# Optimization experiments

Hardware: AMD Instinct MI355X
Metric: run time of the kernel (lower is better)

## Reference

```python
import math
import jax, jax.numpy as jnp
import numpy as np

B, N, C = 4, 2048, 256
KMAX, RATIO, ITERS, H = 1024, 12.0, 3, 4
TAU, SIG_FLOOR, INIT_SIG_MIX, INIT_OFF, JIT = 1.0, 0.03, 0.1, 0.5, 1e-6
W_KL, W_ENT, W_OCC, W_COL = 0.05, 0.0, 0.5, 0.1
K_USE = min(max(1, math.ceil(N / RATIO)), KMAX)  # 171
EPS = 1e-8


def _sym(M):
    return 0.5 * (M + jnp.swapaxes(M, -1, -2))


def _l2n(x):
    return x / jnp.maximum(jnp.linalg.norm(x, axis=-1, keepdims=True), 1e-12)


def _ln(x, g, b):
    m = x.mean(-1, keepdims=True)
    v = ((x - m) ** 2).mean(-1, keepdims=True)
    return (x - m) / jnp.sqrt(v + 1e-5) * g + b


def setup_inputs():
    key = jax.random.key(0)
    ks = jax.random.split(key, 16)
    s = jax.random.normal(ks[0], (B, N, C), jnp.float32)
    mu = jax.random.normal(ks[1], (B, N, 3), jnp.float32)
    # per-point SPD covariances (Sigma must be PSD for the overlap solve)
    L = jax.random.normal(ks[2], (B, N, 3, 3), jnp.float32) * 0.3
    Sigma = L @ jnp.swapaxes(L, -1, -2) + 0.05 * jnp.eye(3, dtype=jnp.float32)
    mask = jnp.ones((B, N), jnp.float32)
    lim = 1.0 / math.sqrt(C)
    u = lambda k, sh: jax.random.uniform(k, sh, jnp.float32, -lim, lim)
    return dict(
        s=s, mu=mu, Sigma=Sigma, mask=mask,
        slot_embed_pool=jax.random.normal(ks[3], (KMAX, C), jnp.float32) * 0.02,
        geo_offsets_pool=jax.random.normal(ks[4], (KMAX, 3), jnp.float32) * 0.5,
        gating_W=u(ks[5], (C, C)), proj_q_W=u(ks[6], (C, C)), proj_k_W=u(ks[7], (C, C)),
        gru_w_ih=u(ks[8], (3 * C, C)), gru_w_hh=u(ks[9], (3 * C, C)),
        gru_b_ih=u(ks[10], (3 * C,)), gru_b_hh=u(ks[11], (3 * C,)),
        ln_g=jnp.ones((C,), jnp.float32), ln_b=jnp.zeros((C,), jnp.float32),
        mlp_w1=u(ks[12], (4 * C, C)), mlp_b1=u(ks[13], (4 * C,)),
        mlp_w2=u(ks[14], (C, 4 * C)), mlp_b2=u(ks[15], (C,)),
        w_geo=jnp.float32(1.0),
        geo_scale_raw=jnp.full((H,), -4.0, jnp.float32),
        geo_bias=jnp.full((H,), -6.0, jnp.float32),
    )


def _forward(s, mu, Sigma, mask, slot_embed_pool, geo_offsets_pool, gating_W,
             proj_q_W, proj_k_W, gru_w_ih, gru_w_hh, gru_b_ih, gru_b_hh,
             ln_g, ln_b, mlp_w1, mlp_b1, mlp_w2, mlp_b2,
             w_geo, geo_scale_raw, geo_bias):
    I3 = jnp.eye(3, dtype=s.dtype)
    m1 = mask[:, :, None]                    # [B,N,1]
    cnt = jnp.maximum(mask.sum(1), EPS)      # [B]

    # ---- slot selection (eval mode: no gate noise, rand_slots=0) ----
    s_global = (s * m1).sum(1) / cnt[:, None]
    q = _l2n(s_global @ gating_W.T)
    kn = _l2n(slot_embed_pool)
    scores = q @ kn.T                        # [B,KMAX]
    idx = jax.lax.top_k(scores, K_USE)[1]    # [B,K]
    slots = slot_embed_pool[idx]             # [B,K,C]
    geo_off = geo_offsets_pool[idx]          # [B,K,3]

    # ---- masked mean/std of mu ----
    mean = (mu * m1).sum(1) / cnt[:, None]   # [B,3]
    dm = mu - mean[:, None, :]
    cov = jnp.einsum('bni,bnj->bij', dm * m1, dm) / cnt[:, None, None]
    cov = _sym(cov)
    std = jnp.sqrt(jnp.maximum(jnp.diagonal(cov, axis1=-2, axis2=-1), EPS))
    std = jnp.maximum(std, SIG_FLOOR)
    mu_k = mean[:, None, :] + geo_off * (INIT_OFF * std[:, None, :])

    Sig_avg = _sym((Sigma * m1[..., None]).sum(1) / cnt[:, None, None])
    Sig_k = jnp.broadcast_to(Sig_avg[:, None] * INIT_SIG_MIX, (B, K_USE, 3, 3))
    Sig_k = Sig_k + (SIG_FLOOR ** 2) * I3 + JIT * I3

    k_sem = s @ proj_k_W.T                   # [B,N,C]
    a_h = jax.nn.softplus(geo_scale_raw)     # [H]
    A = None
    for _ in range(ITERS):
        q_sem = slots @ proj_q_W.T           # [B,K,C]
        logits_sem = jnp.einsum('bnc,bkc->bnk', k_sem, q_sem) / math.sqrt(C)
        delta = mu[:, :, None, :] - mu_k[:, None, :, :]       # [B,N,K,3]
        sig_sum = Sigma[:, :, None] + Sig_k[:, None]          # [B,N,K,3,3]
        sol = jnp.linalg.solve(sig_sum, delta[..., None])[..., 0]
        maha = (delta * sol).sum(-1)
        logdet = jnp.linalg.slogdet(sig_sum)[1]
        G = -0.5 * (maha + logdet)                            # [B,N,K]
        geo = (a_h[None, :, None, None] * G[:, None] + geo_bias[None, :, None, None]).sum(1)
        logits = (logits_sem + w_geo * geo) / max(TAU, 1e-6)
        logits = jnp.where(m1 < 0.5, -1e9, logits)
        A = jax.nn.softmax(logits, axis=-1) * m1              # [B,N,K]
        # moment-matching merge (A already mask-weighted; matches torch A*mask)
        occ = jnp.maximum(A.sum(1), EPS)                      # [B,K]
        mu_k = jnp.einsum('bnk,bni->bki', A, mu) / occ[..., None]
        d = mu[:, :, None, :] - mu_k[:, None, :, :]
        outer = d[..., :, None] * d[..., None, :]             # [B,N,K,3,3]
        Sig_k = (jnp.einsum('bnk,bnij->bkij', A, Sigma)
                 + jnp.einsum('bnk,bnkij->bkij', A, outer)) / occ[:, :, None, None]
        Sig_k = _sym(Sig_k) + max(JIT, 1e-6) * I3
        dg = jnp.diagonal(Sig_k, axis1=-2, axis2=-1)
        dg_f = jnp.maximum(dg, SIG_FLOOR ** 2)
        Sig_k = Sig_k - I3 * dg[..., None, :] + I3 * dg_f[..., None, :]
        Sig_k = _sym(Sig_k) + JIT * I3
        denom = jnp.maximum(A.sum(1), 1e-8)
        slot_in = jnp.einsum('bnk,bnc->bkc', A, s) / denom[..., None]
        # GRU cell
        x = slot_in.reshape(-1, C)
        h = slots.reshape(-1, C)
        gi = x @ gru_w_ih.T + gru_b_ih
        gh = h @ gru_w_hh.T + gru_b_hh
        r = jax.nn.sigmoid(gi[:, :C] + gh[:, :C])
        z = jax.nn.sigmoid(gi[:, C:2 * C] + gh[:, C:2 * C])
        n = jnp.tanh(gi[:, 2 * C:] + r * gh[:, 2 * C:])
        slots = ((1.0 - z) * n + z * h).reshape(B, K_USE, C)
        xm = _ln(slots, ln_g, ln_b)
        slots = slots + (jax.nn.gelu(xm @ mlp_w1.T + mlp_b1, approximate=False) @ mlp_w2.T + mlp_b2)

    # ---- losses ----
    hist = jnp.zeros((KMAX,), jnp.float32).at[idx.reshape(-1)].add(1.0)
    p = hist / jnp.maximum(hist.sum(), 1.0)
    pc = jnp.maximum(p, 1e-8)
    usage_kl = (pc * (jnp.log(pc) - math.log(1.0 / KMAX))).sum()
    usage_neg_ent = (pc * jnp.log(pc)).sum()
    occ2 = (A * m1).sum(1)
    occ2 = occ2 / jnp.maximum(occ2.sum(-1, keepdims=True), 1e-8)
    occ_mse = ((occ2 - 1.0 / K_USE) ** 2).mean()
    X = jnp.swapaxes(A * m1, 1, 2)           # [B,K,N]
    Xn = X / jnp.maximum(jnp.linalg.norm(X, axis=-1, keepdims=True), 1e-8)
    Gm = jnp.einsum('bkn,bln->bkl', Xn, Xn)
    eyeK = jnp.eye(K_USE, dtype=A.dtype)[None]
    off = (Gm - eyeK) * (1.0 - eyeK)
    col = (off ** 2).mean()
    total = W_KL * usage_kl + W_ENT * usage_neg_ent + W_OCC * occ_mse + W_COL * col
    return (A, slots, mu_k, Sig_k, idx, usage_kl, usage_neg_ent, occ_mse, col, total)


def reference(s, mu, Sigma, mask, slot_embed_pool, geo_offsets_pool, gating_W,
              proj_q_W, proj_k_W, gru_w_ih, gru_w_hh, gru_b_ih, gru_b_hh,
              ln_g, ln_b, mlp_w1, mlp_b1, mlp_w2, mlp_b2,
              w_geo, geo_scale_raw, geo_bias):
    return _forward(s, mu, Sigma, mask, slot_embed_pool, geo_offsets_pool, gating_W,
                    proj_q_W, proj_k_W, gru_w_ih, gru_w_hh, gru_b_ih, gru_b_hh,
                    ln_g, ln_b, mlp_w1, mlp_b1, mlp_w2, mlp_b2,
                    w_geo, geo_scale_raw, geo_bias)
```

## Files before the change

kernel.cpp:

```cpp
#include <hip/hip_runtime.h>
#include <math.h>

#define B_ 4
#define N_ 2048
#define C_ 256
#define KMAX_ 1024
#define KU_ 171
#define BK_ 684
#define ITERS_ 3
#define H_ 4
#define EPS_ 1e-8f
#define SIGF_ 0.03f
#define JIT_ 1e-6f
#define LOGKMAX_ 6.93147180559945f

#define WS_CNT 0
#define WS_MUS 4
#define WS_MOS 16
#define WS_SGS 40
#define WS_COLACC 100
#define WS_SSUM 128
#define WS_STATS_BYTES (1152*4)
#define WS_MEAN 1152
#define WS_STD 1164
#define WS_SIGAVG 1176
#define WS_IDXI 1216
#define WS_KSEM 1920
#define WS_QSEM (WS_KSEM+2097152)
#define WS_OCC  (WS_QSEM+175104)
#define WS_PART (WS_OCC+704)
#define WS_W2P  WS_PART
#define WS_GBUF (WS_PART+1400832)
#define WS_ATA  WS_GBUF
#define WS_SNEW (WS_GBUF+700416)
#define WS_XM   (WS_SNEW+175104)
#define WS_HID  (WS_XM+175104)
#define WS_ACPART (WS_HID+700416)
#define WS_QV   (WS_ACPART+28160)
#define WS_SCORE (WS_QV+1024)

#define O_A 0
#define O_SLOTS 1400832
#define O_MUK   1575936
#define O_SIGK  1577988
#define O_IDX   1584144
#define O_KL    1584828
#define O_ENT   1584829
#define O_OCC   1584830
#define O_COL   1584831
#define O_TOT   1584832

__device__ __forceinline__ float wred(float v) {
  #pragma unroll
  for (int i = 32; i; i >>= 1) v += __shfl_xor(v, i);
  return v;
}
__device__ __forceinline__ float wmax(float v) {
  #pragma unroll
  for (int i = 32; i; i >>= 1) v = fmaxf(v, __shfl_xor(v, i));
  return v;
}

__device__ __forceinline__ float blk_red(float v, float* red, int t) {
  red[t] = v; __syncthreads();
  #pragma unroll
  for (int s = 128; s > 0; s >>= 1) {
    if (t < s) red[t] += red[t + s];
    __syncthreads();
  }
  float r = red[0]; __syncthreads();
  return r;
}

__global__ __launch_bounds__(256) void k_stats(const float* __restrict__ s,
    const float* __restrict__ mu, const float* __restrict__ Sigma,
    const float* __restrict__ mask, float* __restrict__ ws) {
  int blk = blockIdx.x; int b = blk / 8; int nc = blk % 8; int t = threadIdx.x;
  int n = nc * 256 + t;
  float m = mask[b * N_ + n];
  const float* mun = mu + ((size_t)(b * N_ + n)) * 3;
  float m0 = mun[0], m1v = mun[1], m2 = mun[2];
  const float* sgn = Sigma + ((size_t)(b * N_ + n)) * 9;
  float sg[9];
  #pragma unroll
  for (int j = 0; j < 9; j++) sg[j] = sgn[j];
  int lane = t & 63;
  float vals[19];
  vals[0] = m; vals[1] = m * m0; vals[2] = m * m1v; vals[3] = m * m2;
  vals[4] = m * m0 * m0; vals[5] = m * m0 * m1v; vals[6] = m * m0 * m2;
  vals[7] = m * m1v * m1v; vals[8] = m * m1v * m2; vals[9] = m * m2 * m2;
  #pragma unroll
  for (int j = 0; j < 9; j++) vals[10 + j] = m * sg[j];
  #pragma unroll
  for (int j = 0; j < 19; j++) {
    float v = wred(vals[j]);
    if (lane == 0) {
      int base = (j == 0) ? WS_CNT + b : (j < 4 ? WS_MUS + b * 3 + (j - 1)
                 : (j < 10 ? WS_MOS + b * 6 + (j - 4) : WS_SGS + b * 9 + (j - 10)));
      atomicAdd(ws + base, v);
    }
  }
  const float* sb = s + ((size_t)b * N_ + nc * 256) * C_;
  const float* mk = mask + b * N_ + nc * 256;
  float sa = 0.f;
  #pragma unroll 4
  for (int nn = 0; nn < 256; nn++) sa += mk[nn] * sb[(size_t)nn * C_ + t];
  atomicAdd(ws + WS_SSUM + b * C_ + t, sa);
}

__global__ __launch_bounds__(64) void k_fin(float* __restrict__ ws) {
  int t = threadIdx.x;
  if (t < B_) {
    int b = t;
    float cnt = fmaxf(ws[WS_CNT + b], EPS_);
    float me[3];
    #pragma unroll
    for (int i = 0; i < 3; i++) { me[i] = ws[WS_MUS + b * 3 + i] / cnt; ws[WS_MEAN + b * 3 + i] = me[i]; }
    const int dg[3] = {0, 3, 5};
    #pragma unroll
    for (int i = 0; i < 3; i++) {
      float cov = ws[WS_MOS + b * 6 + dg[i]] / cnt - me[i] * me[i];
      ws[WS_STD + b * 3 + i] = fmaxf(sqrtf(fmaxf(cov, EPS_)), SIGF_);
    }
    #pragma unroll
    for (int i = 0; i < 3; i++)
      #pragma unroll
      for (int j = 0; j < 3; j++)
        ws[WS_SIGAVG + b * 9 + i * 3 + j] =
            0.5f * (ws[WS_SGS + b * 9 + i * 3 + j] + ws[WS_SGS + b * 9 + j * 3 + i]) / cnt;
  }
}

__global__ __launch_bounds__(256) void k_qv(const float* __restrict__ ws_ssum,
    const float* __restrict__ gW, float* __restrict__ qv_o) {
  int b = blockIdx.x, t = threadIdx.x;
  __shared__ float sb[C_];
  __shared__ float rv[256];
  sb[t] = ws_ssum[b * C_ + t];
  __syncthreads();
  const float4* g4 = (const float4*)(gW + (size_t)t * C_);
  float qr = 0.f;
  #pragma unroll 4
  for (int c4 = 0; c4 < 64; c4++) {
    float4 g = g4[c4];
    qr += sb[c4 * 4] * g.x + sb[c4 * 4 + 1] * g.y + sb[c4 * 4 + 2] * g.z + sb[c4 * 4 + 3] * g.w;
  }
  float n2 = blk_red(qr * qr, rv, t);
  qv_o[b * C_ + t] = qr / fmaxf(sqrtf(n2), 1e-12f);
}

__global__ __launch_bounds__(256) void k_score(const float* __restrict__ qv,
    const float* __restrict__ pool, float* __restrict__ score) {
  int blk = blockIdx.x; int b = blk >> 4; int pc = blk & 15;
  int t = threadIdx.x; int row = pc * 64 + (t >> 2); int q = t & 3;
  __shared__ float qs[C_];
  qs[t] = qv[b * C_ + t];
  __syncthreads();
  const float4* p4 = (const float4*)(pool + (size_t)row * C_ + q * 64);
  float d = 0.f, p2 = 0.f;
  #pragma unroll
  for (int i = 0; i < 16; i++) {
    float4 pv = p4[i];
    int c = q * 64 + i * 4;
    d += qs[c] * pv.x + qs[c + 1] * pv.y + qs[c + 2] * pv.z + qs[c + 3] * pv.w;
    p2 += pv.x * pv.x + pv.y * pv.y + pv.z * pv.z + pv.w * pv.w;
  }
  d += __shfl_xor(d, 1); d += __shfl_xor(d, 2);
  p2 += __shfl_xor(p2, 1); p2 += __shfl_xor(p2, 2);
  if (q == 0) score[b * KMAX_ + row] = d / fmaxf(sqrtf(p2), 1e-12f);
}

__global__ __launch_bounds__(256) void k_sort(const float* __restrict__ score,
    int* __restrict__ idx_o, float* __restrict__ idxf_o) {
  int b = blockIdx.x, t = threadIdx.x;
  __shared__ float val[KMAX_]; __shared__ int id[KMAX_];
  for (int j = t; j < KMAX_; j += 256) { val[j] = score[b * KMAX_ + j]; id[j] = j; }
  __syncthreads();
  for (int kk = 2; kk <= KMAX_; kk <<= 1) {
    for (int j = kk >> 1; j > 0; j >>= 1) {
      for (int i = t; i < KMAX_; i += 256) {
        int ix = i ^ j;
        if (ix > i) {
          float va = val[i], vb = val[ix]; int ia = id[i], ib = id[ix];
          bool bBeforeA = (vb > va) || (vb == va && ib < ia);
          bool up = ((i & kk) == 0);
          if (up == bBeforeA) {
            val[i] = vb; val[ix] = va; id[i] = ib; id[ix] = ia;
          }
        }
      }
      __syncthreads();
    }
  }
  if (t < KU_) {
    idx_o[b * KU_ + t] = id[t];
    idxf_o[b * KU_ + t] = (float)id[t];
  }
}

__global__ __launch_bounds__(256) void k_init(const int* __restrict__ idx,
    const float* __restrict__ pool, const float* __restrict__ geop,
    const float* __restrict__ ws, float* __restrict__ slots,
    float* __restrict__ mu_k, float* __restrict__ sig_k) {
  int blk = blockIdx.x; int b = blk / KU_, k = blk % KU_; int t = threadIdx.x;
  int j = idx[b * KU_ + k];
  slots[((size_t)(b * KU_ + k)) * C_ + t] = pool[(size_t)j * C_ + t];
  if (t < 3) {
    mu_k[(b * KU_ + k) * 3 + t] = ws[WS_MEAN + b * 3 + t] + geop[j * 3 + t] * (0.5f * ws[WS_STD + b * 3 + t]);
  }
  if (t < 9) {
    float v = ws[WS_SIGAVG + b * 9 + t] * 0.1f;
    if (t == 0 || t == 4 || t == 8) v += SIGF_ * SIGF_ + JIT_;
    sig_k[((size_t)(b * KU_ + k)) * 9 + t] = v;
  }
}

template<int ROWS>
__global__ __launch_bounds__(256) void k_gemm_plain(const float* __restrict__ in,
    const float* __restrict__ W, float* __restrict__ out, int IN, int OUT, float scale) {
  extern __shared__ float sm[];
  int t = threadIdx.x; int r0 = blockIdx.x * ROWS;
  int C4 = IN >> 2;
  for (int i = t; i < ROWS * C4; i += 256) {
    int rr = i / C4;
    ((float4*)sm)[i] = ((const float4*)(in + (size_t)(r0 + rr) * IN))[i - rr * C4];
  }
  __syncthreads();
  const float4* W4 = (const float4*)(W + (size_t)t * IN);
  const float4* sm4 = (const float4*)sm;
  float acc[ROWS];
  #pragma unroll
  for (int a = 0; a < ROWS; a++) acc[a] = 0.f;
  for (int c4 = 0; c4 < C4; c4++) {
    float4 wv = W4[c4];
    #pragma unroll
    for (int a = 0; a < ROWS; a++) {
      float4 sv = sm4[a * C4 + c4];
      acc[a] += sv.x * wv.x + sv.y * wv.y + sv.z * wv.z + sv.w * wv.w;
    }
  }
  #pragma unroll
  for (int a = 0; a < ROWS; a++)
    out[(size_t)(r0 + a) * OUT + t] = acc[a] * scale;
}

__global__ __launch_bounds__(256) void k_lgsm(const float* __restrict__ ksem,
    const float* __restrict__ qsem, const float* __restrict__ mu,
    const float* __restrict__ Sigma, const float* __restrict__ mask,
    const float* __restrict__ mu_k, const float* __restrict__ sig_k,
    const float* __restrict__ wgeo, const float* __restrict__ gsr,
    const float* __restrict__ gbias, float* __restrict__ A) {
  __shared__ float ksm[16 * C_];
  __shared__ float Asm[16][172];
  __shared__ float muk[KU_ * 3];
  __shared__ float sgk[KU_ * 6];
  __shared__ float rowd[16][10];
  int blk = blockIdx.x; int b = blk / (N_ / 16); int nt = blk % (N_ / 16);
  int t = threadIdx.x; int r0 = nt * 16;
  for (int i = t; i < 16 * (C_ >> 2); i += 256) {
    int rr = i >> 6;
    ((float4*)ksm)[i] = ((const float4*)(ksem + ((size_t)(b * N_ + r0 + rr)) * C_))[i & 63];
  }
  for (int i = t; i < KU_ * 3; i += 256) muk[i] = mu_k[(size_t)b * KU_ * 3 + i];
  for (int i = t; i < KU_ * 6; i += 256) {
    int k = i / 6, c = i % 6;
    const int map[6] = {0, 1, 2, 4, 5, 8};
    sgk[i] = sig_k[((size_t)(b * KU_ + k)) * 9 + map[c]];
  }
  if (t < 160) {
    int rr = t / 10, c = t % 10;
    int n = r0 + rr;
    float v;
    if (c == 0) v = mask[b * N_ + n];
    else if (c < 4) v = mu[((size_t)(b * N_ + n)) * 3 + (c - 1)];
    else {
      const int map[6] = {0, 1, 2, 4, 5, 8};
      v = Sigma[((size_t)(b * N_ + n)) * 9 + map[c - 4]];
    }
    rowd[rr][c] = v;
  }
  __syncthreads();
  if (t < KU_) {
    const float4* q4 = (const float4*)(qsem + ((size_t)(b * KU_ + t)) * C_);
    const float4* sm4 = (const float4*)ksm;
    float acc[16];
    #pragma unroll
    for (int a = 0; a < 16; a++) acc[a] = 0.f;
    for (int c4 = 0; c4 < 64; c4++) {
      float4 qv = q4[c4];
      #pragma unroll
      for (int a = 0; a < 16; a++) {
        float4 sv = sm4[a * 64 + c4];
        acc[a] += sv.x * qv.x + sv.y * qv.y + sv.z * qv.z + sv.w * qv.w;
      }
    }
    float ah = 0.f, bs = 0.f;
    #pragma unroll
    for (int h = 0; h < H_; h++) {
      float x = gsr[h];
      ah += fmaxf(x, 0.f) + log1pf(expf(-fabsf(x)));
      bs += gbias[h];
    }
    float wg = wgeo[0];
    float mk0 = muk[t * 3], mk1 = muk[t * 3 + 1], mk2 = muk[t * 3 + 2];
    float k00 = sgk[t * 6], k01 = sgk[t * 6 + 1], k02 = sgk[t * 6 + 2];
    float k11 = sgk[t * 6 + 3], k12 = sgk[t * 6 + 4], k22 = sgk[t * 6 + 5];
    #pragma unroll
    for (int a = 0; a < 16; a++) {
      float m = rowd[a][0];
      float d0 = rowd[a][1] - mk0, d1 = rowd[a][2] - mk1, d2 = rowd[a][3] - mk2;
      float s00 = rowd[a][4] + k00, s01 = rowd[a][5] + k01, s02 = rowd[a][6] + k02;
      float s11 = rowd[a][7] + k11, s12 = rowd[a][8] + k12, s22 = rowd[a][9] + k22;
      float c00 = s11 * s22 - s12 * s12;
      float c01 = s02 * s12 - s01 * s22;
      float c02 = s01 * s12 - s02 * s11;
      float det = s00 * c00 + s01 * c01 + s02 * c02;
      float c11 = s00 * s22 - s02 * s02;
      float c12 = s01 * s02 - s00 * s12;
      float c22 = s00 * s11 - s01 * s01;
      float inv = 1.0f / det;
      float x0 = (c00 * d0 + c01 * d1 + c02 * d2) * inv;
      float x1 = (c01 * d0 + c11 * d1 + c12 * d2) * inv;
      float x2 = (c02 * d0 + c12 * d1 + c22 * d2) * inv;
      float maha = d0 * x0 + d1 * x1 + d2 * x2;
      float logdet = logf(fmaxf(det, 1e-30f));
      float G = -0.5f * (maha + logdet);
      float l = acc[a] * 0.0625f + wg * (ah * G + bs);
      if (m < 0.5f) l = -1e9f;
      Asm[a][t] = l;
    }
  }
  __syncthreads();
  int w = t >> 6, lane = t & 63;
  #pragma unroll
  for (int q = 0; q < 4; q++) {
    int a = w * 4 + q;
    float v0 = (lane < KU_) ? Asm[a][lane] : -INFINITY;
    float v1 = (lane + 64 < KU_) ? Asm[a][lane + 64] : -INFINITY;
    float v2 = (lane + 128 < KU_) ? Asm[a][lane + 128] : -INFINITY;
    float mx = wmax(fmaxf(v0, fmaxf(v1, v2)));
    float e0 = (lane < KU_) ? expf(v0 - mx) : 0.f;
    float e1 = (lane + 64 < KU_) ? expf(v1 - mx) : 0.f;
    float e2 = (lane + 128 < KU_) ? expf(v2 - mx) : 0.f;
    float ss = wred(e0 + e1 + e2);
    float scale = rowd[a][0] / ss;
    if (lane < KU_) Asm[a][lane] = e0 * scale;
    if (lane + 64 < KU_) Asm[a][lane + 64] = e1 * scale;
    if (lane + 128 < KU_) Asm[a][lane + 128] = e2 * scale;
  }
  __syncthreads();
  for (int i = t; i < 16 * KU_; i += 256) {
    int a = i / KU_, k = i - a * KU_;
    A[((size_t)(b * N_ + r0 + a)) * KU_ + k] = Asm[a][k];
  }
}

#define AC_NC 4
__global__ __launch_bounds__(256) void k_accum_part(const float* __restrict__ A,
    const float* __restrict__ mu, const float* __restrict__ Sigma,
    float* __restrict__ part) {
  int blk = blockIdx.x;
  int nc = blk & 3; int tmp = blk >> 2; int kt = tmp % 11; int b = tmp / 11;
  int t = threadIdx.x; int nn = t >> 4; int kk = t & 15;
  int k = kt * 16 + kk;
  float S[10];
  #pragma unroll
  for (int i = 0; i < 10; i++) S[i] = 0.f;
  __shared__ float rowd[16][10];
  const int NCH = N_ / AC_NC;
  for (int n0 = nc * NCH; n0 < nc * NCH + NCH; n0 += 16) {
    __syncthreads();
    if (t < 144) {
      int rr = t / 9, c = t % 9;
      int n = n0 + rr;
      float v;
      if (c < 3) v = mu[((size_t)(b * N_ + n)) * 3 + c];
      else {
        const int map[6] = {0, 1, 2, 4, 5, 8};
        v = Sigma[((size_t)(b * N_ + n)) * 9 + map[c - 3]];
      }
      rowd[rr][c] = v;
    }
    float a = (k < KU_) ? A[((size_t)(b * N_ + n0 + nn)) * KU_ + k] : 0.f;
    __syncthreads();
    float m0 = rowd[nn][0], m1 = rowd[nn][1], m2 = rowd[nn][2];
    float g0 = rowd[nn][3], g1 = rowd[nn][4], g2 = rowd[nn][5];
    float g4 = rowd[nn][6], g5 = rowd[nn][7], g8 = rowd[nn][8];
    S[0] += a; S[1] += a * m0; S[2] += a * m1; S[3] += a * m2;
    S[4] += a * (g0 + m0 * m0); S[5] += a * (g1 + m0 * m1); S[6] += a * (g2 + m0 * m2);
    S[7] += a * (g4 + m1 * m1); S[8] += a * (g5 + m1 * m2); S[9] += a * (g8 + m2 * m2);
  }
  #pragma unroll
  for (int i = 0; i < 10; i++) { S[i] += __shfl_xor(S[i], 16); S[i] += __shfl_xor(S[i], 32); }
  __shared__ float red[4][16][10];
  int w = t >> 6, lane = t & 63;
  if (lane < 16) {
    #pragma unroll
    for (int i = 0; i < 10; i++) red[w][lane][i] = S[i];
  }
  __syncthreads();
  if (t < 160) {
    int k2 = t / 10, i = t % 10;
    float v = red[0][k2][i] + red[1][k2][i] + red[2][k2][i] + red[3][k2][i];
    part[(((size_t)nc * B_ + b) * 176 + kt * 16 + k2) * 10 + i] = v;
  }
}

__global__ __launch_bounds__(256) void k_accum_fin(const float* __restrict__ part,
    float* __restrict__ occ, float* __restrict__ mu_k, float* __restrict__ sig_k) {
  int i = blockIdx.x * 256 + threadIdx.x;
  if (i >= B_ * KU_) return;
  int b = i / KU_, k = i % KU_;
  float p[10];
  #pragma unroll
  for (int j = 0; j < 10; j++) {
    float v = 0.f;
    #pragma unroll
    for (int nc = 0; nc < AC_NC; nc++)
      v += part[(((size_t)nc * B_ + b) * 176 + k) * 10 + j];
    p[j] = v;
  }
  float o = p[0];
  occ[b * KU_ + k] = o;
  float oc = fmaxf(o, EPS_);
  float s1x = p[1], s1y = p[2], s1z = p[3];
  float q0 = s1x / oc, q1 = s1y / oc, q2 = s1z / oc;
  mu_k[(b * KU_ + k) * 3 + 0] = q0;
  mu_k[(b * KU_ + k) * 3 + 1] = q1;
  mu_k[(b * KU_ + k) * 3 + 2] = q2;
  float v00 = (p[4] - 2.f * q0 * s1x + o * q0 * q0) / oc + JIT_;
  float v01 = (p[5] - q0 * s1y - s1x * q1 + o * q0 * q1) / oc;
  float v02 = (p[6] - q0 * s1z - s1x * q2 + o * q0 * q2) / oc;
  float v11 = (p[7] - 2.f * q1 * s1y + o * q1 * q1) / oc + JIT_;
  float v12 = (p[8] - q1 * s1z - s1y * q2 + o * q1 * q2) / oc;
  float v22 = (p[9] - 2.f * q2 * s1z + o * q2 * q2) / oc + JIT_;
  v00 = fmaxf(v00, SIGF_ * SIGF_) + JIT_;
  v11 = fmaxf(v11, SIGF_ * SIGF_) + JIT_;
  v22 = fmaxf(v22, SIGF_ * SIGF_) + JIT_;
  float* po = sig_k + ((size_t)(b * KU_ + k)) * 9;
  po[0] = v00; po[1] = v01; po[2] = v02;
  po[3] = v01; po[4] = v11; po[5] = v12;
  po[6] = v02; po[7] = v12; po[8] = v22;
}

__global__ __launch_bounds__(256) void k_atn_s(const float* __restrict__ A,
    const float* __restrict__ X, float* __restrict__ part) {
  int blk = blockIdx.x;
  int nc = blk & 7; int tmp = blk >> 3; int kt = tmp % 11; int b = tmp / 11;
  int t = threadIdx.x; int k0 = kt * 16;
  __shared__ float Ach[64 * 16];
  float acc[16];
  #pragma unroll
  for (int j = 0; j < 16; j++) acc[j] = 0.f;
  for (int n0 = nc * 256; n0 < nc * 256 + 256; n0 += 64) {
    __syncthreads();
    for (int i = t; i < 64 * 16; i += 256) {
      int nn = i >> 4, kk = i & 15; int k = k0 + kk;
      Ach[i] = (k < KU_) ? A[((size_t)(b * N_ + n0 + nn)) * KU_ + k] : 0.f;
    }
    __syncthreads();
    for (int nn = 0; nn < 64; nn++) {
      float xv = X[((size_t)(b * N_ + n0 + nn)) * C_ + t];
      #pragma unroll
      for (int j = 0; j < 16; j++) acc[j] += Ach[(nn << 4) + j] * xv;
    }
  }
  #pragma unroll
  for (int j = 0; j < 16; j++) {
    int k = k0 + j;
    if (k < KU_) part[((size_t)nc * (B_ * KU_) + b * KU_ + k) * C_ + t] = acc[j];
  }
}

__global__ __launch_bounds__(256) void k_atn(const float* __restrict__ A,
    const float* __restrict__ X, float* __restrict__ out, int NX) {
  int blk = blockIdx.x;
  int nc = blk & 7; int tmp = blk >> 3; int kt = tmp % 11; int b = tmp / 11;
  int t = threadIdx.x; int k0 = kt * 16;
  __shared__ float Ach[64 * 16];
  float acc[16];
  #pragma unroll
  for (int j = 0; j < 16; j++) acc[j] = 0.f;
  for (int n0 = nc * 256; n0 < nc * 256 + 256; n0 += 64) {
    __syncthreads();
    for (int i = t; i < 64 * 16; i += 256) {
      int nn = i >> 4, kk = i & 15; int k = k0 + kk;
      Ach[i] = (k < KU_) ? A[((size_t)(b * N_ + n0 + nn)) * KU_ + k] : 0.f;
    }
    __syncthreads();
    if (t < NX) {
      for (int nn = 0; nn < 64; nn++) {
        float xv = X[((size_t)(b * N_ + n0 + nn)) * NX + t];
        #pragma unroll
        for (int j = 0; j < 16; j++) acc[j] += Ach[(nn << 4) + j] * xv;
      }
    }
  }
  if (t < NX) {
    #pragma unroll
    for (int j = 0; j < 16; j++) {
      int k = k0 + j;
      if (k < KU_) atomicAdd(&out[((size_t)(b * KU_ + k)) * NX + t], acc[j]);
    }
  }
}

__global__ __launch_bounds__(256) void k_gg(const float* __restrict__ part,
    const float* __restrict__ occ, const float* __restrict__ slots,
    const float* __restrict__ wih, const float* __restrict__ bih,
    const float* __restrict__ whh, const float* __restrict__ bhh,
    float* __restrict__ gbuf) {
  int p = blockIdx.y; int r0 = blockIdx.x * 8; int t = threadIdx.x;
  __shared__ float sx[8 * C_];
  __shared__ float sh[8 * C_];
  bool needx = (p < 3), needh = (p != 2);
  for (int i = t; i < 8 * C_; i += 256) {
    int rr = i >> 8, c = i & 255;
    int r = r0 + rr;
    if (r < BK_) {
      if (needx) {
        float v = 0.f;
        #pragma unroll
        for (int nc = 0; nc < 8; nc++) v += part[((size_t)nc * BK_ + r) * C_ + c];
        sx[i] = v / fmaxf(occ[r], 1e-8f);
      }
      if (needh) sh[i] = slots[(size_t)r * C_ + c];
    } else {
      if (needx) sx[i] = 0.f;
      if (needh) sh[i] = 0.f;
    }
  }
  __syncthreads();
  int grow = (p == 3) ? 512 + t : ((p == 2) ? 512 + t : p * 256 + t);
  float acc[8];
  #pragma unroll
  for (int a = 0; a < 8; a++) acc[a] = 0.f;
  const float4* sx4 = (const float4*)sx;
  const float4* sh4 = (const float4*)sh;
  if (p < 2) {
    const float4* wi = (const float4*)(wih + (size_t)grow * C_);
    const float4* wh = (const float4*)(whh + (size_t)grow * C_);
    for (int c4 = 0; c4 < 64; c4++) {
      float4 a1 = wi[c4], a2 = wh[c4];
      #pragma unroll
      for (int a = 0; a < 8; a++) {
        float4 xv = sx4[a * 64 + c4], hv = sh4[a * 64 + c4];
        acc[a] += xv.x * a1.x + xv.y * a1.y + xv.z * a1.z + xv.w * a1.w
                + hv.x * a2.x + hv.y * a2.y + hv.z * a2.z + hv.w * a2.w;
      }
    }
  } else if (p == 2) {
    const float4* wi = (const float4*)(wih + (size_t)grow * C_);
    for (int c4 = 0; c4 < 64; c4++) {
      float4 a1 = wi[c4];
      #pragma unroll
      for (int a = 0; a < 8; a++) {
        float4 xv = sx4[a * 64 + c4];
        acc[a] += xv.x * a1.x + xv.y * a1.y + xv.z * a1.z + xv.w * a1.w;
      }
    }
  } else {
    const float4* wh = (const float4*)(whh + (size_t)grow * C_);
    for (int c4 = 0; c4 < 64; c4++) {
      float4 a2 = wh[c4];
      #pragma unroll
      for (int a = 0; a < 8; a++) {
        float4 hv = sh4[a * 64 + c4];
        acc[a] += hv.x * a2.x + hv.y * a2.y + hv.z * a2.z + hv.w * a2.w;
      }
    }
  }
  float bias = (p < 2) ? (bih[grow] + bhh[grow]) : ((p == 2) ? bih[grow] : bhh[grow]);
  #pragma unroll
  for (int a = 0; a < 8; a++) {
    int r = r0 + a;
    if (r < BK_) gbuf[((size_t)p * BK_ + r) * C_ + t] = acc[a] + bias;
  }
}

__global__ __launch_bounds__(256) void k_gru_ln(const float* __restrict__ gbuf,
    const float* __restrict__ slots, const float* __restrict__ lng,
    const float* __restrict__ lnb, float* __restrict__ snew, float* __restrict__ xm) {
  int r = blockIdx.x; int t = threadIdx.x;
  float gr = gbuf[((size_t)0 * BK_ + r) * C_ + t];
  float gz = gbuf[((size_t)1 * BK_ + r) * C_ + t];
  float gi = gbuf[((size_t)2 * BK_ + r) * C_ + t];
  float gh = gbuf[((size_t)3 * BK_ + r) * C_ + t];
  float rg = 1.f / (1.f + expf(-gr));
  float z = 1.f / (1.f + expf(-gz));
  float n = tanhf(gi + rg * gh);
  float h = slots[(size_t)r * C_ + t];
  float sn = (1.f - z) * n + z * h;
  snew[(size_t)r * C_ + t] = sn;
  __shared__ float reda[4], redb[4];
  int w = t >> 6, lane = t & 63;
  float sum = wred(sn);
  if (lane == 0) reda[w] = sum;
  __syncthreads();
  float mean = (reda[0] + reda[1] + reda[2] + reda[3]) * (1.f / 256.f);
  float d = sn - mean;
  float vs = wred(d * d);
  if (lane == 0) redb[w] = vs;
  __syncthreads();
  float var = (redb[0] + redb[1] + redb[2] + redb[3]) * (1.f / 256.f);
  xm[(size_t)r * C_ + t] = d * rsqrtf(var + 1e-5f) * lng[t] + lnb[t];
}

__global__ __launch_bounds__(256) void k_w1(const float* __restrict__ xm,
    const float* __restrict__ w1p, const float* __restrict__ b1p,
    float* __restrict__ hid) {
  int r0 = blockIdx.x * 4; int t = threadIdx.x; int oc = blockIdx.y * 256 + t;
  __shared__ float sm[4 * C_];
  for (int i = t; i < 4 * 64; i += 256) {
    int rr = i >> 6;
    ((float4*)sm)[i] = ((const float4*)(xm + (size_t)(r0 + rr) * C_))[i & 63];
  }
  __syncthreads();
  const float4* W4 = (const float4*)(w1p + (size_t)oc * C_);
  const float4* sm4 = (const float4*)sm;
  float acc[4] = {0, 0, 0, 0};
  for (int c4 = 0; c4 < 64; c4++) {
    float4 wv = W4[c4];
    #pragma unroll
    for (int a = 0; a < 4; a++) {
      float4 sv = sm4[a * 64 + c4];
      acc[a] += sv.x * wv.x + sv.y * wv.y + sv.z * wv.z + sv.w * wv.w;
    }
  }
  float bb = b1p[oc];
  #pragma unroll
  for (int a = 0; a < 4; a++) {
    float v = acc[a] + bb;
    hid[(size_t)(r0 + a) * 1024 + oc] = 0.5f * v * (1.f + erff(v * 0.70710678118654752f));
  }
}

__global__ __launch_bounds__(256) void k_w2p(const float* __restrict__ hid,
    const float* __restrict__ w2p, float* __restrict__ w2part) {
  int r0 = blockIdx.x * 4; int kc = blockIdx.y; int t = threadIdx.x;
  __shared__ float sm[4 * C_];
  for (int i = t; i < 4 * 64; i += 256) {
    int rr = i >> 6;
    ((float4*)sm)[i] = ((const float4*)(hid + (size_t)(r0 + rr) * 1024 + kc * 256))[i & 63];
  }
  __syncthreads();
  const float4* W4 = (const float4*)(w2p + (size_t)t * 1024 + kc * 256);
  const float4* sm4 = (const float4*)sm;
  float acc[4] = {0, 0, 0, 0};
  for (int c4 = 0; c4 < 64; c4++) {
    float4 wv = W4[c4];
    #pragma unroll
    for (int a = 0; a < 4; a++) {
      float4 sv = sm4[a * 64 + c4];
      acc[a] += sv.x * wv.x + sv.y * wv.y + sv.z * wv.z + sv.w * wv.w;
    }
  }
  #pragma unroll
  for (int a = 0; a < 4; a++)
    w2part[((size_t)kc * BK_ + r0 + a) * C_ + t] = acc[a];
}

__global__ __launch_bounds__(256) void k_qsemf(const float* __restrict__ snew,
    const float* __restrict__ w2part, const float* __restrict__ b2p,
    const float* __restrict__ qWp, float* __restrict__ slots,
    float* __restrict__ qsem) {
  int r0 = blockIdx.x * 4; int t = threadIdx.x;
  __shared__ float sfin[4 * C_];
  for (int i = t; i < 4 * C_; i += 256) {
    int rr = i >> 8, c = i & 255;
    int r = r0 + rr;
    float v = snew[(size_t)r * C_ + c] + b2p[c];
    #pragma unroll
    for (int kc = 0; kc < 4; kc++) v += w2part[((size_t)kc * BK_ + r) * C_ + c];
    sfin[i] = v;
    slots[(size_t)r * C_ + c] = v;
  }
  __syncthreads();
  const float4* qr = (const float4*)(qWp + (size_t)t * C_);
  const float4* s4 = (const float4*)sfin;
  float o[4] = {0, 0, 0, 0};
  for (int c4 = 0; c4 < 64; c4++) {
    float4 wv = qr[c4];
    #pragma unroll
    for (int a = 0; a < 4; a++) {
      float4 xv = s4[a * 64 + c4];
      o[a] += xv.x * wv.x + xv.y * wv.y + xv.z * wv.z + xv.w * wv.w;
    }
  }
  #pragma unroll
  for (int a = 0; a < 4; a++)
    qsem[(size_t)(r0 + a) * C_ + t] = o[a];
}

__global__ __launch_bounds__(256) void k_hist(const int* __restrict__ idx,
    float* __restrict__ okl, float* __restrict__ oent) {
  __shared__ float hist[KMAX_];
  int t = threadIdx.x;
  for (int i = t; i < KMAX_; i += 256) hist[i] = 0.f;
  __syncthreads();
  for (int i = t; i < B_ * KU_; i += 256) atomicAdd(&hist[idx[i]], 1.0f);
  __syncthreads();
  float kl = 0.f, ent = 0.f;
  const float tot = (float)(B_ * KU_);
  for (int i = t; i < KMAX_; i += 256) {
    float pc = fmaxf(hist[i] / tot, 1e-8f);
    float lp = logf(pc);
    kl += pc * (lp + LOGKMAX_);
    ent += pc * lp;
  }
  __shared__ float red[256];
  kl = blk_red(kl, red, t); ent = blk_red(ent, red, t);
  if (t == 0) { okl[0] = kl; oent[0] = ent; }
}

__global__ __launch_bounds__(256) void k_occmse(const float* __restrict__ occ,
    float* __restrict__ out) {
  __shared__ float so[B_ * KU_];
  int t = threadIdx.x;
  for (int i = t; i < B_ * KU_; i += 256) so[i] = occ[i];
  __syncthreads();
  __shared__ float red[256];
  __shared__ float bsum[B_];
  for (int b = 0; b < B_; b++) {
    float s = 0.f;
    for (int i = t; i < KU_; i += 256) s += so[b * KU_ + i];
    s = blk_red(s, red, t);
    if (t == 0) bsum[b] = fmaxf(s, 1e-8f);
    __syncthreads();
  }
  float acc = 0.f;
  const float invK = 1.0f / (float)KU_;
  for (int i = t; i < B_ * KU_; i += 256) {
    int b = i / KU_;
    float v = so[i] / bsum[b] - invK;
    acc += v * v;
  }
  acc = blk_red(acc, red, t);
  if (t == 0) out[0] = acc / (float)(B_ * KU_);
}

__global__ __launch_bounds__(256) void k_colpart(const float* __restrict__ AtA,
    float* __restrict__ colacc) {
  int blk = blockIdx.x; int b = blk / KU_, k = blk % KU_; int t = threadIdx.x;
  float acc = 0.f;
  if (t < KU_ && t != k) {
    float dk = AtA[((size_t)(b * KU_ + k)) * KU_ + k];
    float dt = AtA[((size_t)(b * KU_ + t)) * KU_ + t];
    float v  = AtA[((size_t)(b * KU_ + k)) * KU_ + t];
    float gm = v / (fmaxf(sqrtf(dk), 1e-8f) * fmaxf(sqrtf(dt), 1e-8f));
    acc = gm * gm;
  }
  float v = wred(acc);
  __shared__ float p[4];
  if ((t & 63) == 0) p[t >> 6] = v;
  __syncthreads();
  if (t == 0) atomicAdd(colacc, p[0] + p[1] + p[2] + p[3]);
}

__global__ void k_colfin(const float* __restrict__ colacc,
    const float* __restrict__ okl, const float* __restrict__ oent,
    const float* __restrict__ oocc, float* __restrict__ ocol, float* __restrict__ otot) {
  float col = colacc[0] / (float)(B_ * KU_ * KU_);
  ocol[0] = col;
  otot[0] = 0.05f * okl[0] + 0.0f * oent[0] + 0.5f * oocc[0] + 0.1f * col;
}

extern "C" void kernel_launch(void* const* d_in, const int* in_sizes, int n_in,
                              void* d_out_v, int out_size, void* d_ws, size_t ws_size,
                              hipStream_t stream) {
  const float* s     = (const float*)d_in[0];
  const float* mu    = (const float*)d_in[1];
  const float* Sigma = (const float*)d_in[2];
  const float* mask  = (const float*)d_in[3];
  const float* pool  = (const float*)d_in[4];
  const float* geop  = (const float*)d_in[5];
  const float* gW    = (const float*)d_in[6];
  const float* qW    = (const float*)d_in[7];
  const float* kW    = (const float*)d_in[8];
  const float* wih   = (const float*)d_in[9];
  const float* whh   = (const float*)d_in[10];
  const float* bih   = (const float*)d_in[11];
  const float* bhh   = (const float*)d_in[12];
  const float* lng   = (const float*)d_in[13];
  const float* lnb   = (const float*)d_in[14];
  const float* w1    = (const float*)d_in[15];
  const float* b1    = (const float*)d_in[16];
  const float* w2    = (const float*)d_in[17];
  const float* b2    = (const float*)d_in[18];
  const float* wgeo  = (const float*)d_in[19];
  const float* gsr   = (const float*)d_in[20];
  const float* gbias = (const float*)d_in[21];

  float* out = (float*)d_out_v;
  float* A     = out + O_A;
  float* slots = out + O_SLOTS;
  float* muk   = out + O_MUK;
  float* sigk  = out + O_SIGK;
  float* idxf  = out + O_IDX;
  float* okl   = out + O_KL;
  float* oent  = out + O_ENT;
  float* oocc  = out + O_OCC;
  float* ocol  = out + O_COL;
  float* otot  = out + O_TOT;

  float* ws = (float*)d_ws;
  int*   idxi   = (int*)(ws + WS_IDXI);
  float* ksem   = ws + WS_KSEM;
  float* qsem   = ws + WS_QSEM;
  float* occ    = ws + WS_OCC;
  float* atpart = ws + WS_PART;
  float* gbuf   = ws + WS_GBUF;
  float* snew   = ws + WS_SNEW;
  float* xm     = ws + WS_XM;
  float* hid    = ws + WS_HID;
  float* w2part = ws + WS_W2P;
  float* acpart = ws + WS_ACPART;
  float* ata    = ws + WS_ATA;
  float* colacc = ws + WS_COLACC;

  hipMemsetAsync(ws, 0, WS_STATS_BYTES, stream);
  k_stats<<<B_ * 8, 256, 0, stream>>>(s, mu, Sigma, mask, ws);
  k_fin<<<1, 64, 0, stream>>>(ws);
  k_qv<<<B_, 256, 0, stream>>>(ws + WS_SSUM, gW, ws + WS_QV);
  k_score<<<B_ * 16, 256, 0, stream>>>(ws + WS_QV, pool, ws + WS_SCORE);
  k_sort<<<B_, 256, 0, stream>>>(ws + WS_SCORE, idxi, idxf);
  k_init<<<B_ * KU_, 256, 0, stream>>>(idxi, pool, geop, ws, slots, muk, sigk);

  k_gemm_plain<8><<<1024, 256, 8 * C_ * 4, stream>>>(s, kW, ksem, C_, C_, 1.0f);
  k_gemm_plain<4><<<171, 256, 4 * C_ * 4, stream>>>(slots, qW, qsem, C_, C_, 1.0f);

  for (int it = 0; it < ITERS_; ++it) {
    k_lgsm<<<B_ * (N_ / 16), 256, 0, stream>>>(ksem, qsem, mu, Sigma, mask,
                                               muk, sigk, wgeo, gsr, gbias, A);
    k_accum_part<<<B_ * 11 * AC_NC, 256, 0, stream>>>(A, mu, Sigma, acpart);
    k_accum_fin<<<3, 256, 0, stream>>>(acpart, occ, muk, sigk);
    k_atn_s<<<B_ * 11 * 8, 256, 0, stream>>>(A, s, atpart);
    k_gg<<<dim3(86, 4), 256, 0, stream>>>(atpart, occ, slots, wih, bih, whh, bhh, gbuf);
    k_gru_ln<<<BK_, 256, 0, stream>>>(gbuf, slots, lng, lnb, snew, xm);
    k_w1<<<dim3(171, 4), 256, 0, stream>>>(xm, w1, b1, hid);
    k_w2p<<<dim3(171, 4), 256, 0, stream>>>(hid, w2, w2part);
    k_qsemf<<<171, 256, 0, stream>>>(snew, w2part, b2, qW, slots, qsem);
  }

  hipMemsetAsync(ata, 0, (size_t)B_ * KU_ * KU_ * 4, stream);
  k_atn<<<B_ * 11 * 8, 256, 0, stream>>>(A, A, ata, KU_);
  k_colpart<<<B_ * KU_, 256, 0, stream>>>(ata, colacc);
  k_hist<<<1, 256, 0, stream>>>(idxi, okl, oent);
  k_occmse<<<1, 256, 0, stream>>>(occ, oocc);
  k_colfin<<<1, 1, 0, stream>>>(colacc, okl, oent, oocc, ocol, otot);
}
```

Before: 877.4 us.

## Fuse per-iteration kernels and halve row tile in attention softmax

Merges several small kernels to cut launch count. k_fin goes into k_qv, and k_accum_part and k_atn_s become one k_amoms launch with block ranges for each role. k_accum_fin is folded into extra blocks of k_gg, with occupancy recomputed locally, and GRU+LayerNorm is fused into the W1 GEMM, which removes the xm buffer. The hist and occ-MSE kernels become one two-block launch. The lgsm row tile drops from 16 to 8 rows to create more blocks, at the cost of reloading qsem twice as often. The W1 fusion also recomputes the GRU and LayerNorm in each of the four y-blocks.

Measured after the change: 786.5 us. 1.12x faster.

```diff
diff --git a/kernel.cpp b/kernel.cpp
--- a/kernel.cpp
+++ b/kernel.cpp
@@ -33,8 +33,7 @@
 #define WS_GBUF (WS_PART+1400832)
 #define WS_ATA  WS_GBUF
 #define WS_SNEW (WS_GBUF+700416)
-#define WS_XM   (WS_SNEW+175104)
-#define WS_HID  (WS_XM+175104)
+#define WS_HID  (WS_SNEW+175104)
 #define WS_ACPART (WS_HID+700416)
 #define WS_QV   (WS_ACPART+28160)
 #define WS_SCORE (WS_QV+1024)
@@ -108,36 +107,32 @@
   atomicAdd(ws + WS_SSUM + b * C_ + t, sa);
 }
 
-__global__ __launch_bounds__(64) void k_fin(float* __restrict__ ws) {
-  int t = threadIdx.x;
-  if (t < B_) {
-    int b = t;
-    float cnt = fmaxf(ws[WS_CNT + b], EPS_);
-    float me[3];
-    #pragma unroll
-    for (int i = 0; i < 3; i++) { me[i] = ws[WS_MUS + b * 3 + i] / cnt; ws[WS_MEAN + b * 3 + i] = me[i]; }
-    const int dg[3] = {0, 3, 5};
-    #pragma unroll
-    for (int i = 0; i < 3; i++) {
-      float cov = ws[WS_MOS + b * 6 + dg[i]] / cnt - me[i] * me[i];
-      ws[WS_STD + b * 3 + i] = fmaxf(sqrtf(fmaxf(cov, EPS_)), SIGF_);
-    }
-    #pragma unroll
-    for (int i = 0; i < 3; i++)
-      #pragma unroll
-      for (int j = 0; j < 3; j++)
-        ws[WS_SIGAVG + b * 9 + i * 3 + j] =
-            0.5f * (ws[WS_SGS + b * 9 + i * 3 + j] + ws[WS_SGS + b * 9 + j * 3 + i]) / cnt;
-  }
-}
-
-__global__ __launch_bounds__(256) void k_qv(const float* __restrict__ ws_ssum,
+__global__ __launch_bounds__(256) void k_qv(float* __restrict__ ws,
     const float* __restrict__ gW, float* __restrict__ qv_o) {
   int b = blockIdx.x, t = threadIdx.x;
   __shared__ float sb[C_];
   __shared__ float rv[256];
-  sb[t] = ws_ssum[b * C_ + t];
-  __syncthreads();
+  sb[t] = ws[WS_SSUM + b * C_ + t];
+  __syncthreads();
+  if (blockIdx.x == 0 && t < B_) {
+    int bb = t;
+    float cnt = fmaxf(ws[WS_CNT + bb], EPS_);
+    float me[3];
+    #pragma unroll
+    for (int i = 0; i < 3; i++) { me[i] = ws[WS_MUS + bb * 3 + i] / cnt; ws[WS_MEAN + bb * 3 + i] = me[i]; }
+    const int dg[3] = {0, 3, 5};
+    #pragma unroll
+    for (int i = 0; i < 3; i++) {
+      float cov = ws[WS_MOS + bb * 6 + dg[i]] / cnt - me[i] * me[i];
+      ws[WS_STD + bb * 3 + i] = fmaxf(sqrtf(fmaxf(cov, EPS_)), SIGF_);
+    }
+    #pragma unroll
+    for (int i = 0; i < 3; i++)
+      #pragma unroll
+      for (int j = 0; j < 3; j++)
+        ws[WS_SIGAVG + bb * 9 + i * 3 + j] =
+            0.5f * (ws[WS_SGS + bb * 9 + i * 3 + j] + ws[WS_SGS + bb * 9 + j * 3 + i]) / cnt;
+  }
   const float4* g4 = (const float4*)(gW + (size_t)t * C_);
   float qr = 0.f;
   #pragma unroll 4
@@ -244,20 +239,21 @@
     out[(size_t)(r0 + a) * OUT + t] = acc[a] * scale;
 }
 
+#define LG_R 8
 __global__ __launch_bounds__(256) void k_lgsm(const float* __restrict__ ksem,
     const float* __restrict__ qsem, const float* __restrict__ mu,
     const float* __restrict__ Sigma, const float* __restrict__ mask,
     const float* __restrict__ mu_k, const float* __restrict__ sig_k,
     const float* __restrict__ wgeo, const float* __restrict__ gsr,
     const float* __restrict__ gbias, float* __restrict__ A) {
-  __shared__ float ksm[16 * C_];
-  __shared__ float Asm[16][172];
+  __shared__ float ksm[LG_R * C_];
+  __shared__ float Asm[LG_R][172];
   __shared__ float muk[KU_ * 3];
   __shared__ float sgk[KU_ * 6];
-  __shared__ float rowd[16][10];
-  int blk = blockIdx.x; int b = blk / (N_ / 16); int nt = blk % (N_ / 16);
-  int t = threadIdx.x; int r0 = nt * 16;
-  for (int i = t; i < 16 * (C_ >> 2); i += 256) {
+  __shared__ float rowd[LG_R][10];
+  int blk = blockIdx.x; int b = blk / (N_ / LG_R); int nt = blk % (N_ / LG_R);
+  int t = threadIdx.x; int r0 = nt * LG_R;
+  for (int i = t; i < LG_R * (C_ >> 2); i += 256) {
     int rr = i >> 6;
     ((float4*)ksm)[i] = ((const float4*)(ksem + ((size_t)(b * N_ + r0 + rr)) * C_))[i & 63];
   }
@@ -267,7 +263,7 @@
     const int map[6] = {0, 1, 2, 4, 5, 8};
     sgk[i] = sig_k[((size_t)(b * KU_ + k)) * 9 + map[c]];
   }
-  if (t < 160) {
+  if (t < LG_R * 10) {
     int rr = t / 10, c = t % 10;
     int n = r0 + rr;
     float v;
@@ -283,13 +279,13 @@
   if (t < KU_) {
     const float4* q4 = (const float4*)(qsem + ((size_t)(b * KU_ + t)) * C_);
     const float4* sm4 = (const float4*)ksm;
-    float acc[16];
-    #pragma unroll
-    for (int a = 0; a < 16; a++) acc[a] = 0.f;
+    float acc[LG_R];
+    #pragma unroll
+    for (int a = 0; a < LG_R; a++) acc[a] = 0.f;
     for (int c4 = 0; c4 < 64; c4++) {
       float4 qv = q4[c4];
       #pragma unroll
-      for (int a = 0; a < 16; a++) {
+      for (int a = 0; a < LG_R; a++) {
         float4 sv = sm4[a * 64 + c4];
         acc[a] += sv.x * qv.x + sv.y * qv.y + sv.z * qv.z + sv.w * qv.w;
       }
@@ -306,7 +302,7 @@
     float k00 = sgk[t * 6], k01 = sgk[t * 6 + 1], k02 = sgk[t * 6 + 2];
     float k11 = sgk[t * 6 + 3], k12 = sgk[t * 6 + 4], k22 = sgk[t * 6 + 5];
     #pragma unroll
-    for (int a = 0; a < 16; a++) {
+    for (int a = 0; a < LG_R; a++) {
       float m = rowd[a][0];
       float d0 = rowd[a][1] - mk0, d1 = rowd[a][2] - mk1, d2 = rowd[a][3] - mk2;
       float s00 = rowd[a][4] + k00, s01 = rowd[a][5] + k01, s02 = rowd[a][6] + k02;
@@ -333,8 +329,8 @@
   __syncthreads();
   int w = t >> 6, lane = t & 63;
   #pragma unroll
-  for (int q = 0; q < 4; q++) {
-    int a = w * 4 + q;
+  for (int q = 0; q < 2; q++) {
+    int a = w * 2 + q;
     float v0 = (lane < KU_) ? Asm[a][lane] : -INFINITY;
     float v1 = (lane + 64 < KU_) ? Asm[a][lane + 64] : -INFINITY;
     float v2 = (lane + 128 < KU_) ? Asm[a][lane + 128] : -INFINITY;
@@ -349,171 +345,155 @@
     if (lane + 128 < KU_) Asm[a][lane + 128] = e2 * scale;
   }
   __syncthreads();
-  for (int i = t; i < 16 * KU_; i += 256) {
+  for (int i = t; i < LG_R * KU_; i += 256) {
     int a = i / KU_, k = i - a * KU_;
     A[((size_t)(b * N_ + r0 + a)) * KU_ + k] = Asm[a][k];
   }
 }
 
 #define AC_NC 4
-__global__ __launch_bounds__(256) void k_accum_part(const float* __restrict__ A,
+__global__ __launch_bounds__(256) void k_amoms(const float* __restrict__ A,
     const float* __restrict__ mu, const float* __restrict__ Sigma,
-    float* __restrict__ part) {
-  int blk = blockIdx.x;
-  int nc = blk & 3; int tmp = blk >> 2; int kt = tmp % 11; int b = tmp / 11;
-  int t = threadIdx.x; int nn = t >> 4; int kk = t & 15;
-  int k = kt * 16 + kk;
-  float S[10];
-  #pragma unroll
-  for (int i = 0; i < 10; i++) S[i] = 0.f;
-  __shared__ float rowd[16][10];
-  const int NCH = N_ / AC_NC;
-  for (int n0 = nc * NCH; n0 < nc * NCH + NCH; n0 += 16) {
+    const float* __restrict__ s, float* __restrict__ acpart,
+    float* __restrict__ atpart) {
+  __shared__ float shm[1024];
+  __shared__ float red2[4][16][10];
+  int t = threadIdx.x;
+  if (blockIdx.x < 176) {
+    int blk = blockIdx.x;
+    int nc = blk & 3; int tmp = blk >> 2; int kt = tmp % 11; int b = tmp / 11;
+    int nn = t >> 4; int kk = t & 15;
+    int k = kt * 16 + kk;
+    float S[10];
+    #pragma unroll
+    for (int i = 0; i < 10; i++) S[i] = 0.f;
+    float (*rowd)[10] = (float(*)[10])shm;
+    const int NCH = N_ / AC_NC;
+    for (int n0 = nc * NCH; n0 < nc * NCH + NCH; n0 += 16) {
+      __syncthreads();
+      if (t < 144) {
+        int rr = t / 9, c = t % 9;
+        int n = n0 + rr;
+        float v;
+        if (c < 3) v = mu[((size_t)(b * N_ + n)) * 3 + c];
+        else {
+          const int map[6] = {0, 1, 2, 4, 5, 8};
+          v = Sigma[((size_t)(b * N_ + n)) * 9 + map[c - 3]];
+        }
+        rowd[rr][c] = v;
+      }
+      float a = (k < KU_) ? A[((size_t)(b * N_ + n0 + nn)) * KU_ + k] : 0.f;
+      __syncthreads();
+      float m0 = rowd[nn][0], m1 = rowd[nn][1], m2 = rowd[nn][2];
+      float g0 = rowd[nn][3], g1 = rowd[nn][4], g2 = rowd[nn][5];
+      float g4 = rowd[nn][6], g5 = rowd[nn][7], g8 = rowd[nn][8];
+      S[0] += a; S[1] += a * m0; S[2] += a * m1; S[3] += a * m2;
+      S[4] += a * (g0 + m0 * m0); S[5] += a * (g1 + m0 * m1); S[6] += a * (g2 + m0 * m2);
+      S[7] += a * (g4 + m1 * m1); S[8] += a * (g5 + m1 * m2); S[9] += a * (g8 + m2 * m2);
+    }
+    #pragma unroll
+    for (int i = 0; i < 10; i++) { S[i] += __shfl_xor(S[i], 16); S[i] += __shfl_xor(S[i], 32); }
+    int w = t >> 6, lane = t & 63;
+    if (lane < 16) {
+      #pragma unroll
+      for (int i = 0; i < 10; i++) red2[w][lane][i] = S[i];
+    }
     __syncthreads();
-    if (t < 144) {
-      int rr = t / 9, c = t % 9;
-      int n = n0 + rr;
-      float v;
-      if (c < 3) v = mu[((size_t)(b * N_ + n)) * 3 + c];
-      else {
-        const int map[6] = {0, 1, 2, 4, 5, 8};
-        v = Sigma[((size_t)(b * N_ + n)) * 9 + map[c - 3]];
-      }
-      rowd[rr][c] = v;
-    }
-    float a = (k < KU_) ? A[((size_t)(b * N_ + n0 + nn)) * KU_ + k] : 0.f;
-    __syncthreads();
-    float m0 = rowd[nn][0], m1 = rowd[nn][1], m2 = rowd[nn][2];
-    float g0 = rowd[nn][3], g1 = rowd[nn][4], g2 = rowd[nn][5];
-    float g4 = rowd[nn][6], g5 = rowd[nn][7], g8 = rowd[nn][8];
-    S[0] += a; S[1] += a * m0; S[2] += a * m1; S[3] += a * m2;
-    S[4] += a * (g0 + m0 * m0); S[5] += a * (g1 + m0 * m1); S[6] += a * (g2 + m0 * m2);
-    S[7] += a * (g4 + m1 * m1); S[8] += a * (g5 + m1 * m2); S[9] += a * (g8 + m2 * m2);
-  }
-  #pragma unroll
-  for (int i = 0; i < 10; i++) { S[i] += __shfl_xor(S[i], 16); S[i] += __shfl_xor(S[i], 32); }
-  __shared__ float red[4][16][10];
-  int w = t >> 6, lane = t & 63;
-  if (lane < 16) {
-    #pragma unroll
-    for (int i = 0; i < 10; i++) red[w][lane][i] = S[i];
-  }
-  __syncthreads();
-  if (t < 160) {
-    int k2 = t / 10, i = t % 10;
-    float v = red[0][k2][i] + red[1][k2][i] + red[2][k2][i] + red[3][k2][i];
-    part[(((size_t)nc * B_ + b) * 176 + kt * 16 + k2) * 10 + i] = v;
-  }
-}
-
-__global__ __launch_bounds__(256) void k_accum_fin(const float* __restrict__ part,
-    float* __restrict__ occ, float* __restrict__ mu_k, float* __restrict__ sig_k) {
-  int i = blockIdx.x * 256 + threadIdx.x;
-  if (i >= B_ * KU_) return;
-  int b = i / KU_, k = i % KU_;
-  float p[10];
-  #pragma unroll
-  for (int j = 0; j < 10; j++) {
-    float v = 0.f;
-    #pragma unroll
-    for (int nc = 0; nc < AC_NC; nc++)
-      v += part[(((size_t)nc * B_ + b) * 176 + k) * 10 + j];
-    p[j] = v;
-  }
-  float o = p[0];
-  occ[b * KU_ + k] = o;
-  float oc = fmaxf(o, EPS_);
-  float s1x = p[1], s1y = p[2], s1z = p[3];
-  float q0 = s1x / oc, q1 = s1y / oc, q2 = s1z / oc;
-  mu_k[(b * KU_ + k) * 3 + 0] = q0;
-  mu_k[(b * KU_ + k) * 3 + 1] = q1;
-  mu_k[(b * KU_ + k) * 3 + 2] = q2;
-  float v00 = (p[4] - 2.f * q0 * s1x + o * q0 * q0) / oc + JIT_;
-  float v01 = (p[5] - q0 * s1y - s1x * q1 + o * q0 * q1) / oc;
-  float v02 = (p[6] - q0 * s1z - s1x * q2 + o * q0 * q2) / oc;
-  float v11 = (p[7] - 2.f * q1 * s1y + o * q1 * q1) / oc + JIT_;
-  float v12 = (p[8] - q1 * s1z - s1y * q2 + o * q1 * q2) / oc;
-  float v22 = (p[9] - 2.f * q2 * s1z + o * q2 * q2) / oc + JIT_;
-  v00 = fmaxf(v00, SIGF_ * SIGF_) + JIT_;
-  v11 = fmaxf(v11, SIGF_ * SIGF_) + JIT_;
-  v22 = fmaxf(v22, SIGF_ * SIGF_) + JIT_;
-  float* po = sig_k + ((size_t)(b * KU_ + k)) * 9;
-  po[0] = v00; po[1] = v01; po[2] = v02;
-  po[3] = v01; po[4] = v11; po[5] = v12;
-  po[6] = v02; po[7] = v12; po[8] = v22;
-}
-
-__global__ __launch_bounds__(256) void k_atn_s(const float* __restrict__ A,
-    const float* __restrict__ X, float* __restrict__ part) {
-  int blk = blockIdx.x;
-  int nc = blk & 7; int tmp = blk >> 3; int kt = tmp % 11; int b = tmp / 11;
-  int t = threadIdx.x; int k0 = kt * 16;
-  __shared__ float Ach[64 * 16];
-  float acc[16];
-  #pragma unroll
-  for (int j = 0; j < 16; j++) acc[j] = 0.f;
-  for (int n0 = nc * 256; n0 < nc * 256 + 256; n0 += 64) {
-    __syncthreads();
-    for (int i = t; i < 64 * 16; i += 256) {
-      int nn = i >> 4, kk = i & 15; int k = k0 + kk;
-      Ach[i] = (k < KU_) ? A[((size_t)(b * N_ + n0 + nn)) * KU_ + k] : 0.f;
-    }
-    __syncthreads();
-    for (int nn = 0; nn < 64; nn++) {
-      float xv = X[((size_t)(b * N_ + n0 + nn)) * C_ + t];
-      #pragma unroll
-      for (int j = 0; j < 16; j++) acc[j] += Ach[(nn << 4) + j] * xv;
-    }
-  }
-  #pragma unroll
-  for (int j = 0; j < 16; j++) {
-    int k = k0 + j;
-    if (k < KU_) part[((size_t)nc * (B_ * KU_) + b * KU_ + k) * C_ + t] = acc[j];
-  }
-}
-
-__global__ __launch_bounds__(256) void k_atn(const float* __restrict__ A,
-    const float* __restrict__ X, float* __restrict__ out, int NX) {
-  int blk = blockIdx.x;
-  int nc = blk & 7; int tmp = blk >> 3; int kt = tmp % 11; int b = tmp / 11;
-  int t = threadIdx.x; int k0 = kt * 16;
-  __shared__ float Ach[64 * 16];
-  float acc[16];
-  #pragma unroll
-  for (int j = 0; j < 16; j++) acc[j] = 0.f;
-  for (int n0 = nc * 256; n0 < nc * 256 + 256; n0 += 64) {
-    __syncthreads();
-    for (int i = t; i < 64 * 16; i += 256) {
-      int nn = i >> 4, kk = i & 15; int k = k0 + kk;
-      Ach[i] = (k < KU_) ? A[((size_t)(b * N_ + n0 + nn)) * KU_ + k] : 0.f;
-    }
-    __syncthreads();
-    if (t < NX) {
+    if (t < 160) {
+      int k2 = t / 10, i = t % 10;
+      float v = red2[0][k2][i] + red2[1][k2][i] + red2[2][k2][i] + red2[3][k2][i];
+      acpart[(((size_t)nc * B_ + b) * 176 + kt * 16 + k2) * 10 + i] = v;
+    }
+  } else {
+    int blk = blockIdx.x - 176;
+    int nc = blk & 7; int tmp = blk >> 3; int kt = tmp % 11; int b = tmp / 11;
+    int k0 = kt * 16;
+    float* Ach = shm;
+    float acc[16];
+    #pragma unroll
+    for (int j = 0; j < 16; j++) acc[j] = 0.f;
+    for (int n0 = nc * 256; n0 < nc * 256 + 256; n0 += 64) {
+      __syncthreads();
+      for (int i = t; i < 64 * 16; i += 256) {
+        int nn = i >> 4, kk = i & 15; int k = k0 + kk;
+        Ach[i] = (k < KU_) ? A[((size_t)(b * N_ + n0 + nn)) * KU_ + k] : 0.f;
+      }
+      __syncthreads();
       for (int nn = 0; nn < 64; nn++) {
-        float xv = X[((size_t)(b * N_ + n0 + nn)) * NX + t];
+        float xv = s[((size_t)(b * N_ + n0 + nn)) * C_ + t];
         #pragma unroll
         for (int j = 0; j < 16; j++) acc[j] += Ach[(nn << 4) + j] * xv;
       }
     }
-  }
-  if (t < NX) {
     #pragma unroll
     for (int j = 0; j < 16; j++) {
       int k = k0 + j;
-      if (k < KU_) atomicAdd(&out[((size_t)(b * KU_ + k)) * NX + t], acc[j]);
-    }
-  }
-}
-
-__global__ __launch_bounds__(256) void k_gg(const float* __restrict__ part,
-    const float* __restrict__ occ, const float* __restrict__ slots,
+      if (k < KU_) atpart[((size_t)nc * (B_ * BK_ / 4) + b * KU_ + k) * C_ + t] = acc[j];
+    }
+  }
+}
+
+__global__ __launch_bounds__(256) void k_gg(const float* __restrict__ atpart,
+    const float* __restrict__ acpart, const float* __restrict__ slots,
     const float* __restrict__ wih, const float* __restrict__ bih,
     const float* __restrict__ whh, const float* __restrict__ bhh,
-    float* __restrict__ gbuf) {
-  int p = blockIdx.y; int r0 = blockIdx.x * 8; int t = threadIdx.x;
+    float* __restrict__ gbuf, float* __restrict__ occ,
+    float* __restrict__ mu_k, float* __restrict__ sig_k) {
+  int t = threadIdx.x;
+  if (blockIdx.x >= 86) {
+    if (blockIdx.y != 0) return;
+    int i = (blockIdx.x - 86) * 256 + t;
+    if (i >= B_ * KU_) return;
+    int b = i / KU_, k = i % KU_;
+    float p[10];
+    #pragma unroll
+    for (int j = 0; j < 10; j++) {
+      float v = 0.f;
+      #pragma unroll
+      for (int nc = 0; nc < AC_NC; nc++)
+        v += acpart[(((size_t)nc * B_ + b) * 176 + k) * 10 + j];
+      p[j] = v;
+    }
+    float o = p[0];
+    occ[b * KU_ + k] = o;
+    float oc = fmaxf(o, EPS_);
+    float s1x = p[1], s1y = p[2], s1z = p[3];
+    float q0 = s1x / oc, q1 = s1y / oc, q2 = s1z / oc;
+    mu_k[(b * KU_ + k) * 3 + 0] = q0;
+    mu_k[(b * KU_ + k) * 3 + 1] = q1;
+    mu_k[(b * KU_ + k) * 3 + 2] = q2;
+    float v00 = (p[4] - 2.f * q0 * s1x + o * q0 * q0) / oc + JIT_;
+    float v01 = (p[5] - q0 * s1y - s1x * q1 + o * q0 * q1) / oc;
+    float v02 = (p[6] - q0 * s1z - s1x * q2 + o * q0 * q2) / oc;
+    float v11 = (p[7] - 2.f * q1 * s1y + o * q1 * q1) / oc + JIT_;
+    float v12 = (p[8] - q1 * s1z - s1y * q2 + o * q1 * q2) / oc;
+    float v22 = (p[9] - 2.f * q2 * s1z + o * q2 * q2) / oc + JIT_;
+    v00 = fmaxf(v00, SIGF_ * SIGF_) + JIT_;
+    v11 = fmaxf(v11, SIGF_ * SIGF_) + JIT_;
+    v22 = fmaxf(v22, SIGF_ * SIGF_) + JIT_;
+    float* po = sig_k + ((size_t)(b * KU_ + k)) * 9;
+    po[0] = v00; po[1] = v01; po[2] = v02;
+    po[3] = v01; po[4] = v11; po[5] = v12;
+    po[6] = v02; po[7] = v12; po[8] = v22;
+    return;
+  }
+  int p = blockIdx.y; int r0 = blockIdx.x * 8;
   __shared__ float sx[8 * C_];
   __shared__ float sh[8 * C_];
+  __shared__ float socc[8];
   bool needx = (p < 3), needh = (p != 2);
+  if (t < 8) {
+    int r = r0 + t;
+    float o = 0.f;
+    if (r < BK_) {
+      int b = r / KU_, k = r % KU_;
+      #pragma unroll
+      for (int nc = 0; nc < AC_NC; nc++)
+        o += acpart[(((size_t)nc * B_ + b) * 176 + k) * 10];
+    }
+    socc[t] = fmaxf(o, 1e-8f);
+  }
+  __syncthreads();
   for (int i = t; i < 8 * C_; i += 256) {
     int rr = i >> 8, c = i & 255;
     int r = r0 + rr;
@@ -521,8 +501,8 @@
       if (needx) {
         float v = 0.f;
         #pragma unroll
-        for (int nc = 0; nc < 8; nc++) v += part[((size_t)nc * BK_ + r) * C_ + c];
-        sx[i] = v / fmaxf(occ[r], 1e-8f);
+        for (int nc = 0; nc < 8; nc++) v += atpart[((size_t)nc * BK_ + r) * C_ + c];
+        sx[i] = v / socc[rr];
       }
       if (needh) sh[i] = slots[(size_t)r * C_ + c];
     } else {
@@ -531,7 +511,7 @@
     }
   }
   __syncthreads();
-  int grow = (p == 3) ? 512 + t : ((p == 2) ? 512 + t : p * 256 + t);
+  int grow = (p >= 2) ? 512 + t : p * 256 + t;
   float acc[8];
   #pragma unroll
   for (int a = 0; a < 8; a++) acc[a] = 0.f;
@@ -578,46 +558,47 @@
   }
 }
 
-__global__ __launch_bounds__(256) void k_gru_ln(const float* __restrict__ gbuf,
+__global__ __launch_bounds__(256) void k_w1ln(const float* __restrict__ gbuf,
     const float* __restrict__ slots, const float* __restrict__ lng,
-    const float* __restrict__ lnb, float* __restrict__ snew, float* __restrict__ xm) {
-  int r = blockIdx.x; int t = threadIdx.x;
-  float gr = gbuf[((size_t)0 * BK_ + r) * C_ + t];
-  float gz = gbuf[((size_t)1 * BK_ + r) * C_ + t];
-  float gi = gbuf[((size_t)2 * BK_ + r) * C_ + t];
-  float gh = gbuf[((size_t)3 * BK_ + r) * C_ + t];
-  float rg = 1.f / (1.f + expf(-gr));
-  float z = 1.f / (1.f + expf(-gz));
-  float n = tanhf(gi + rg * gh);
-  float h = slots[(size_t)r * C_ + t];
-  float sn = (1.f - z) * n + z * h;
-  snew[(size_t)r * C_ + t] = sn;
-  __shared__ float reda[4], redb[4];
-  int w = t >> 6, lane = t & 63;
-  float sum = wred(sn);
-  if (lane == 0) reda[w] = sum;
-  __syncthreads();
-  float mean = (reda[0] + reda[1] + reda[2] + reda[3]) * (1.f / 256.f);
-  float d = sn - mean;
-  float vs = wred(d * d);
-  if (lane == 0) redb[w] = vs;
-  __syncthreads();
-  float var = (redb[0] + redb[1] + redb[2] + redb[3]) * (1.f / 256.f);
-  xm[(size_t)r * C_ + t] = d * rsqrtf(var + 1e-5f) * lng[t] + lnb[t];
-}
-
-__global__ __launch_bounds__(256) void k_w1(const float* __restrict__ xm,
-    const float* __restrict__ w1p, const float* __restrict__ b1p,
+    const float* __restrict__ lnb, const float* __restrict__ w1p,
+    const float* __restrict__ b1p, float* __restrict__ snew,
     float* __restrict__ hid) {
   int r0 = blockIdx.x * 4; int t = threadIdx.x; int oc = blockIdx.y * 256 + t;
-  __shared__ float sm[4 * C_];
-  for (int i = t; i < 4 * 64; i += 256) {
-    int rr = i >> 6;
-    ((float4*)sm)[i] = ((const float4*)(xm + (size_t)(r0 + rr) * C_))[i & 63];
+  __shared__ float ssn[4 * C_];
+  __shared__ float sxm[4 * C_];
+  bool wr = (blockIdx.y == 0);
+  for (int i = t; i < 4 * C_; i += 256) {
+    int rr = i >> 8, c = i & 255;
+    int r = r0 + rr;
+    float gr = gbuf[((size_t)0 * BK_ + r) * C_ + c];
+    float gz = gbuf[((size_t)1 * BK_ + r) * C_ + c];
+    float gi = gbuf[((size_t)2 * BK_ + r) * C_ + c];
+    float gh = gbuf[((size_t)3 * BK_ + r) * C_ + c];
+    float rg = 1.f / (1.f + expf(-gr));
+    float z = 1.f / (1.f + expf(-gz));
+    float n = tanhf(gi + rg * gh);
+    float h = slots[(size_t)r * C_ + c];
+    float sn = (1.f - z) * n + z * h;
+    ssn[i] = sn;
+    if (wr) snew[(size_t)r * C_ + c] = sn;
+  }
+  __syncthreads();
+  {
+    int w = t >> 6, lane = t & 63;
+    float x0 = ssn[w * 256 + lane], x1 = ssn[w * 256 + lane + 64];
+    float x2 = ssn[w * 256 + lane + 128], x3 = ssn[w * 256 + lane + 192];
+    float mean = wred(x0 + x1 + x2 + x3) * (1.f / 256.f);
+    float d0 = x0 - mean, d1 = x1 - mean, d2 = x2 - mean, d3 = x3 - mean;
+    float var = wred(d0 * d0 + d1 * d1 + d2 * d2 + d3 * d3) * (1.f / 256.f);
+    float rstd = rsqrtf(var + 1e-5f);
+    sxm[w * 256 + lane]       = d0 * rstd * lng[lane]       + lnb[lane];
+    sxm[w * 256 + lane + 64]  = d1 * rstd * lng[lane + 64]  + lnb[lane + 64];
+    sxm[w * 256 + lane + 128] = d2 * rstd * lng[lane + 128] + lnb[lane + 128];
+    sxm[w * 256 + lane + 192] = d3 * rstd * lng[lane + 192] + lnb[lane + 192];
   }
   __syncthreads();
   const float4* W4 = (const float4*)(w1p + (size_t)oc * C_);
-  const float4* sm4 = (const float4*)sm;
+  const float4* sm4 = (const float4*)sxm;
   float acc[4] = {0, 0, 0, 0};
   for (int c4 = 0; c4 < 64; c4++) {
     float4 wv = W4[c4];
@@ -692,51 +673,81 @@
     qsem[(size_t)(r0 + a) * C_ + t] = o[a];
 }
 
-__global__ __launch_bounds__(256) void k_hist(const int* __restrict__ idx,
-    float* __restrict__ okl, float* __restrict__ oent) {
-  __shared__ float hist[KMAX_];
+__global__ __launch_bounds__(256) void k_atn(const float* __restrict__ A,
+    const float* __restrict__ X, float* __restrict__ out, int NX) {
+  int blk = blockIdx.x;
+  int nc = blk & 7; int tmp = blk >> 3; int kt = tmp % 11; int b = tmp / 11;
+  int t = threadIdx.x; int k0 = kt * 16;
+  __shared__ float Ach[64 * 16];
+  float acc[16];
+  #pragma unroll
+  for (int j = 0; j < 16; j++) acc[j] = 0.f;
+  for (int n0 = nc * 256; n0 < nc * 256 + 256; n0 += 64) {
+    __syncthreads();
+    for (int i = t; i < 64 * 16; i += 256) {
+      int nn = i >> 4, kk = i & 15; int k = k0 + kk;
+      Ach[i] = (k < KU_) ? A[((size_t)(b * N_ + n0 + nn)) * KU_ + k] : 0.f;
+    }
+    __syncthreads();
+    if (t < NX) {
+      for (int nn = 0; nn < 64; nn++) {
+        float xv = X[((size_t)(b * N_ + n0 + nn)) * NX + t];
+        #pragma unroll
+        for (int j = 0; j < 16; j++) acc[j] += Ach[(nn << 4) + j] * xv;
+      }
+    }
+  }
+  if (t < NX) {
+    #pragma unroll
+    for (int j = 0; j < 16; j++) {
+      int k = k0 + j;
+      if (k < KU_) atomicAdd(&out[((size_t)(b * KU_ + k)) * NX + t], acc[j]);
+    }
+  }
+}
+
+__global__ __launch_bounds__(256) void k_histocc(const int* __restrict__ idx,
+    const float* __restrict__ occ, float* __restrict__ okl,
+    float* __restrict__ oent, float* __restrict__ oocc) {
   int t = threadIdx.x;
-  for (int i = t; i < KMAX_; i += 256) hist[i] = 0.f;
-  __syncthreads();
-  for (int i = t; i < B_ * KU_; i += 256) atomicAdd(&hist[idx[i]], 1.0f);
-  __syncthreads();
-  float kl = 0.f, ent = 0.f;
-  const float tot = (float)(B_ * KU_);
-  for (int i = t; i < KMAX_; i += 256) {
-    float pc = fmaxf(hist[i] / tot, 1e-8f);
-    float lp = logf(pc);
-    kl += pc * (lp + LOGKMAX_);
-    ent += pc * lp;
-  }
+  __shared__ float buf[KMAX_];
   __shared__ float red[256];
-  kl = blk_red(kl, red, t); ent = blk_red(ent, red, t);
-  if (t == 0) { okl[0] = kl; oent[0] = ent; }
-}
-
-__global__ __launch_bounds__(256) void k_occmse(const float* __restrict__ occ,
-    float* __restrict__ out) {
-  __shared__ float so[B_ * KU_];
-  int t = threadIdx.x;
-  for (int i = t; i < B_ * KU_; i += 256) so[i] = occ[i];
-  __syncthreads();
-  __shared__ float red[256];
-  __shared__ float bsum[B_];
-  for (int b = 0; b < B_; b++) {
-    float s = 0.f;
-    for (int i = t; i < KU_; i += 256) s += so[b * KU_ + i];
-    s = blk_red(s, red, t);
-    if (t == 0) bsum[b] = fmaxf(s, 1e-8f);
+  if (blockIdx.x == 0) {
+    for (int i = t; i < KMAX_; i += 256) buf[i] = 0.f;
     __syncthreads();
-  }
-  float acc = 0.f;
-  const float invK = 1.0f / (float)KU_;
-  for (int i = t; i < B_ * KU_; i += 256) {
-    int b = i / KU_;
-    float v = so[i] / bsum[b] - invK;
-    acc += v * v;
-  }
-  acc = blk_red(acc, red, t);
-  if (t == 0) out[0] = acc / (float)(B_ * KU_);
+    for (int i = t; i < B_ * KU_; i += 256) atomicAdd(&buf[idx[i]], 1.0f);
+    __syncthreads();
+    float kl = 0.f, ent = 0.f;
+    const float tot = (float)(B_ * KU_);
+    for (int i = t; i < KMAX_; i += 256) {
+      float pc = fmaxf(buf[i] / tot, 1e-8f);
+      float lp = logf(pc);
+      kl += pc * (lp + LOGKMAX_);
+      ent += pc * lp;
+    }
+    kl = blk_red(kl, red, t); ent = blk_red(ent, red, t);
+    if (t == 0) { okl[0] = kl; oent[0] = ent; }
+  } else {
+    for (int i = t; i < B_ * KU_; i += 256) buf[i] = occ[i];
+    __syncthreads();
+    __shared__ float bsum[B_];
+    for (int b = 0; b < B_; b++) {
+      float s = 0.f;
+      for (int i = t; i < KU_; i += 256) s += buf[b * KU_ + i];
+      s = blk_red(s, red, t);
+      if (t == 0) bsum[b] = fmaxf(s, 1e-8f);
+      __syncthreads();
+    }
+    float acc = 0.f;
+    const float invK = 1.0f / (float)KU_;
+    for (int i = t; i < B_ * KU_; i += 256) {
+      int b = i / KU_;
+      float v = buf[i] / bsum[b] - invK;
+      acc += v * v;
+    }
+    acc = blk_red(acc, red, t);
+    if (t == 0) oocc[0] = acc / (float)(B_ * KU_);
+  }
 }
 
 __global__ __launch_bounds__(256) void k_colpart(const float* __restrict__ AtA,
@@ -811,7 +822,6 @@
   float* atpart = ws + WS_PART;
   float* gbuf   = ws + WS_GBUF;
   float* snew   = ws + WS_SNEW;
-  float* xm     = ws + WS_XM;
   float* hid    = ws + WS_HID;
   float* w2part = ws + WS_W2P;
   float* acpart = ws + WS_ACPART;
@@ -820,8 +830,7 @@
 
   hipMemsetAsync(ws, 0, WS_STATS_BYTES, stream);
   k_stats<<<B_ * 8, 256, 0, stream>>>(s, mu, Sigma, mask, ws);
-  k_fin<<<1, 64, 0, stream>>>(ws);
-  k_qv<<<B_, 256, 0, stream>>>(ws + WS_SSUM, gW, ws + WS_QV);
+  k_qv<<<B_, 256, 0, stream>>>(ws, gW, ws + WS_QV);
   k_score<<<B_ * 16, 256, 0, stream>>>(ws + WS_QV, pool, ws + WS_SCORE);
   k_sort<<<B_, 256, 0, stream>>>(ws + WS_SCORE, idxi, idxf);
   k_init<<<B_ * KU_, 256, 0, stream>>>(idxi, pool, geop, ws, slots, muk, sigk);
@@ -830,14 +839,12 @@
   k_gemm_plain<4><<<171, 256, 4 * C_ * 4, stream>>>(slots, qW, qsem, C_, C_, 1.0f);
 
   for (int it = 0; it < ITERS_; ++it) {
-    k_lgsm<<<B_ * (N_ / 16), 256, 0, stream>>>(ksem, qsem, mu, Sigma, mask,
-                                               muk, sigk, wgeo, gsr, gbias, A);
-    k_accum_part<<<B_ * 11 * AC_NC, 256, 0, stream>>>(A, mu, Sigma, acpart);
-    k_accum_fin<<<3, 256, 0, stream>>>(acpart, occ, muk, sigk);
-    k_atn_s<<<B_ * 11 * 8, 256, 0, stream>>>(A, s, atpart);
-    k_gg<<<dim3(86, 4), 256, 0, stream>>>(atpart, occ, slots, wih, bih, whh, bhh, gbuf);
-    k_gru_ln<<<BK_, 256, 0, stream>>>(gbuf, slots, lng, lnb, snew, xm);
-    k_w1<<<dim3(171, 4), 256, 0, stream>>>(xm, w1, b1, hid);
+    k_lgsm<<<B_ * (N_ / LG_R), 256, 0, stream>>>(ksem, qsem, mu, Sigma, mask,
+                                                 muk, sigk, wgeo, gsr, gbias, A);
+    k_amoms<<<176 + 352, 256, 0, stream>>>(A, mu, Sigma, s, acpart, atpart);
+    k_gg<<<dim3(89, 4), 256, 0, stream>>>(atpart, acpart, slots, wih, bih, whh, bhh,
+                                          gbuf, occ, muk, sigk);
+    k_w1ln<<<dim3(171, 4), 256, 0, stream>>>(gbuf, slots, lng, lnb, w1, b1, snew, hid);
     k_w2p<<<dim3(171, 4), 256, 0, stream>>>(hid, w2, w2part);
     k_qsemf<<<171, 256, 0, stream>>>(snew, w2part, b2, qW, slots, qsem);
   }
@@ -845,7 +852,6 @@
   hipMemsetAsync(ata, 0, (size_t)B_ * KU_ * KU_ * 4, stream);
   k_atn<<<B_ * 11 * 8, 256, 0, stream>>>(A, A, ata, KU_);
   k_colpart<<<B_ * KU_, 256, 0, stream>>>(ata, colacc);
-  k_hist<<<1, 256, 0, stream>>>(idxi, okl, oent);
-  k_occmse<<<1, 256, 0, stream>>>(occ, oocc);
+  k_histocc<<<2, 256, 0, stream>>>(idxi, occ, okl, oent, oocc);
   k_colfin<<<1, 1, 0, stream>>>(colacc, okl, oent, oocc, ocol, otot);
 }
```
